# Optimization experiments

Hardware: AMD Instinct MI355X
Metric: run time of the kernel (lower is better)

The kernel has to match this reference:

```python
import jax, jax.numpy as jnp
import numpy as np

DIM = 1024
HIDDEN = 4096
N_EXPERTS = 8
K = 2
TEMP = 1.0


def setup_inputs() -> dict:
    key = jax.random.key(0)
    ks = jax.random.split(key, 7)
    s = 0.02
    x = jax.random.normal(ks[0], (4, 2048, DIM), dtype=jnp.float32)
    router_w = jax.random.normal(ks[1], (N_EXPERTS, DIM), dtype=jnp.float32) * s
    router_b = jnp.zeros((N_EXPERTS,), dtype=jnp.float32)
    # Expert(dim, hidden, 'swiglu'): fc1: dim -> 2*hidden, fc2: hidden -> dim
    w1 = jax.random.normal(ks[2], (N_EXPERTS, 2 * HIDDEN, DIM), dtype=jnp.float32) * s
    b1 = jnp.zeros((N_EXPERTS, 2 * HIDDEN), dtype=jnp.float32)
    w2 = jax.random.normal(ks[3], (N_EXPERTS, DIM, HIDDEN), dtype=jnp.float32) * s
    b2 = jnp.zeros((N_EXPERTS, DIM), dtype=jnp.float32)
    return {"x": x, "router_w": router_w, "router_b": router_b,
            "w1": w1, "b1": b1, "w2": w2, "b2": b2}


def _expert_ffn(xf, wa, ba, wb, bb):
    # xf: [T, dim]; swiglu FFN
    h = xf @ wa.T + ba                       # [T, 2*hidden]
    h1, h2 = jnp.split(h, 2, axis=-1)
    h = jax.nn.silu(h1) * h2                 # [T, hidden]
    return h @ wb.T + bb                     # [T, dim]


def reference(x, router_w, router_b, w1, b1, w2, b2):
    b, t, d = x.shape
    logits = (x @ router_w.T + router_b) / TEMP          # [b, t, E]
    topk_val, topk_idx = jax.lax.top_k(logits, K)        # [b, t, K]
    weights = jax.nn.softmax(topk_val, axis=-1)          # [b, t, K]

    xf = x.reshape(-1, d)                                # [T, dim]
    # Compute every expert on all tokens (dense reference for irregular dispatch)
    outs = jax.vmap(_expert_ffn, in_axes=(None, 0, 0, 0, 0))(xf, w1, b1, w2, b2)  # [E, T, dim]
    outs = jnp.transpose(outs, (1, 0, 2))                # [T, E, dim]

    idx = topk_idx.reshape(-1, K)                        # [T, K]
    gathered = jnp.take_along_axis(outs, idx[:, :, None], axis=1)  # [T, K, dim]
    combined = (gathered * weights.reshape(-1, K, 1)).sum(axis=1)  # [T, dim]
    return combined.reshape(b, t, d)
```

## Files before the change

### kernel.cpp

```cpp
#include <hip/hip_runtime.h>

#define T_TOK 8192
#define DIMX 1024
#define HID 4096
#define NE 8
#define TP (T_TOK * 2)
#define PADR 128
#define BK 64

typedef unsigned short ushort_t;
typedef __attribute__((ext_vector_type(4))) float f32x4;
typedef __attribute__((ext_vector_type(8))) short bf16x8;
typedef __attribute__((ext_vector_type(8))) unsigned short u16x8;

__device__ __forceinline__ ushort_t f2bf(float f) {
    unsigned u = __float_as_uint(f);
    u += 0x7FFFu + ((u >> 16) & 1u);
    return (ushort_t)(u >> 16);
}
__device__ __forceinline__ float b2f(ushort_t h) {
    return __uint_as_float(((unsigned)h) << 16);
}

__device__ __forceinline__ void gload_lds16(const void* g, void* l) {
    __builtin_amdgcn_global_load_lds((const __attribute__((address_space(1))) void*)g,
                                     (__attribute__((address_space(3))) void*)l, 16, 0, 0);
}

__device__ __forceinline__ f32x4 mfma16(bf16x8 a, bf16x8 b, f32x4 c) {
    return __builtin_amdgcn_mfma_f32_16x16x32_bf16(a, b, c, 0, 0, 0);
}


__global__ __launch_bounds__(256) void router_kernel(
    const float* __restrict__ x, const float* __restrict__ rw, const float* __restrict__ rb,
    int* __restrict__ topk_idx, float* __restrict__ topk_w)
{
    __shared__ float s_rw[NE * DIMX];
    int tid = threadIdx.x;
    for (int i = tid * 4; i < NE * DIMX; i += 1024) {
        float4 v = *(const float4*)(rw + i);
        *(float4*)(s_rw + i) = v;
    }
    __syncthreads();
    int lane = tid & 63, wid = tid >> 6;
    int t = blockIdx.x * 4 + wid;
    const float* xr = x + (size_t)t * DIMX;
    float acc[NE];
#pragma unroll
    for (int e = 0; e < NE; e++) acc[e] = 0.f;
    for (int j = 0; j < DIMX; j += 64) {
        float xv = xr[j + lane];
#pragma unroll
        for (int e = 0; e < NE; e++) acc[e] += xv * s_rw[e * DIMX + j + lane];
    }
#pragma unroll
    for (int e = 0; e < NE; e++) {
#pragma unroll
        for (int off = 32; off > 0; off >>= 1) acc[e] += __shfl_xor(acc[e], off, 64);
    }
    if (lane == 0) {
        float v[NE];
#pragma unroll
        for (int e = 0; e < NE; e++) v[e] = acc[e] + rb[e];
        int i0 = 0; float b0 = v[0];
#pragma unroll
        for (int e = 1; e < NE; e++) if (v[e] > b0) { b0 = v[e]; i0 = e; }
        int i1 = -1; float b1v = -1e30f;
#pragma unroll
        for (int e = 0; e < NE; e++) if (e != i0 && v[e] > b1v) { b1v = v[e]; i1 = e; }
        float ex = __expf(b1v - b0);
        float inv = 1.f / (1.f + ex);
        topk_idx[t * 2]     = i0;  topk_idx[t * 2 + 1] = i1;
        topk_w[t * 2]       = inv; topk_w[t * 2 + 1]   = ex * inv;
    }
}

__global__ __launch_bounds__(256) void prefix_kernel(
    const int* __restrict__ topk_idx, int* __restrict__ counts,
    int* __restrict__ offsets, int* __restrict__ cursor)
{
    __shared__ int hist[NE * 256];
    int tid = threadIdx.x;
    int loc[NE];
#pragma unroll
    for (int e = 0; e < NE; e++) loc[e] = 0;
    for (int i = tid; i < TP; i += 256) loc[topk_idx[i]]++;
#pragma unroll
    for (int e = 0; e < NE; e++) hist[e * 256 + tid] = loc[e];
    __syncthreads();
    if (tid < NE) {
        int s = 0;
        for (int j = 0; j < 256; j++) s += hist[tid * 256 + j];
        counts[tid] = s;
        cursor[tid] = 0;
    }
    __syncthreads();
    if (tid == 0) {
        int s = 0;
        for (int e = 0; e < NE; e++) { offsets[e] = s; s += counts[e]; }
    }
}

__global__ __launch_bounds__(256) void sg_kernel(
    const float* __restrict__ x, const int* __restrict__ topk_idx,
    const float* __restrict__ topk_w, const int* __restrict__ offsets,
    int* __restrict__ cursor, ushort_t* __restrict__ Xp,
    float* __restrict__ w_of, int* __restrict__ slot_of)
{
    __shared__ int s_pos[2];
    int t = blockIdx.x;
    if (threadIdx.x == 0) {
        int e0 = topk_idx[2 * t], e1 = topk_idx[2 * t + 1];
        int p0 = offsets[e0] + atomicAdd(&cursor[e0], 1);
        int p1 = offsets[e1] + atomicAdd(&cursor[e1], 1);
        s_pos[0] = p0; s_pos[1] = p1;
        w_of[p0] = topk_w[2 * t]; w_of[p1] = topk_w[2 * t + 1];
        slot_of[2 * t] = p0; slot_of[2 * t + 1] = p1;
    }
    __syncthreads();
    int p0 = s_pos[0], p1 = s_pos[1];
    int i = threadIdx.x;
    float4 v = ((const float4*)(x + (size_t)t * DIMX))[i];
    ushort4 o = make_ushort4(f2bf(v.x), f2bf(v.y), f2bf(v.z), f2bf(v.w));
    ((ushort4*)(Xp + (size_t)p0 * DIMX))[i] = o;
    ((ushort4*)(Xp + (size_t)p1 * DIMX))[i] = o;
}


__global__ __launch_bounds__(256) void cvt_kernel(
    const float* __restrict__ w1, ushort_t* __restrict__ w1d,
    const float* __restrict__ w2, ushort_t* __restrict__ w2d)
{
    const int n8_w1 = NE * 2 * HID * DIMX / 8;
    const int n8_tot = n8_w1 + NE * DIMX * HID / 8;
    int stride = gridDim.x * 256;
    for (int i = blockIdx.x * 256 + threadIdx.x; i < n8_tot; i += stride) {
        const float* src; ushort_t* dst; int j;
        if (i < n8_w1) { src = w1; dst = w1d; j = i; }
        else           { src = w2; dst = w2d; j = i - n8_w1; }
        float4 a = ((const float4*)src)[j * 2];
        float4 b = ((const float4*)src)[j * 2 + 1];
        u16x8 o = { f2bf(a.x), f2bf(a.y), f2bf(a.z), f2bf(a.w),
                    f2bf(b.x), f2bf(b.y), f2bf(b.z), f2bf(b.w) };
        ((u16x8*)dst)[j] = o;
    }
}

__global__ __launch_bounds__(256, 2) void fc1_kernel(
    const ushort_t* __restrict__ Xp, const ushort_t* __restrict__ w1b,
    const float* __restrict__ b1,
    const int* __restrict__ counts, const int* __restrict__ offsets,
    ushort_t* __restrict__ H, const int nt0)
{
    const int e = blockIdx.z, mt = blockIdx.y, nt = blockIdx.x + nt0;
    const int cnt = counts[e];
    if (mt * 128 >= cnt) return;
    const int base = offsets[e] + mt * 128;
    int rows_valid = cnt - mt * 128; if (rows_valid > 128) rows_valid = 128;

    __shared__ ushort_t As[128 * BK];
    __shared__ ushort_t Bs1[64 * BK];
    __shared__ ushort_t Bs2[64 * BK];

    const int tid = threadIdx.x, lane = tid & 63, wid = tid >> 6;
    const int wave_m = wid >> 1, wave_n = wid & 1;

    const ushort_t* Ag  = Xp + (size_t)base * DIMX;
    const ushort_t* B1g = w1b + ((size_t)e * 2 * HID + (size_t)nt * 64) * DIMX;
    const ushort_t* B2g = B1g + (size_t)HID * DIMX;

    const ushort_t* agp[4]; ushort_t* alp[4];
#pragma unroll
    for (int i = 0; i < 4; i++) {
        int s = wid * 4 + i;
        int r = s * 8 + (lane >> 3);
        int c = (lane & 7) ^ (r & 7);
        agp[i] = Ag + (size_t)r * DIMX + c * 8;
        alp[i] = As + s * 512 + lane * 8;
    }
    const ushort_t* bgp[4]; ushort_t* blp[4];
#pragma unroll
    for (int i = 0; i < 2; i++) {
        int s = wid * 2 + i;
        int r = s * 8 + (lane >> 3);
        int c = (lane & 7) ^ (r & 7);
        bgp[i]     = B1g + (size_t)r * DIMX + c * 8;
        blp[i]     = Bs1 + s * 512 + lane * 8;
        bgp[2 + i] = B2g + (size_t)r * DIMX + c * 8;
        blp[2 + i] = Bs2 + s * 512 + lane * 8;
    }

    f32x4 acc1[4][2], acc2[4][2];
#pragma unroll
    for (int mf = 0; mf < 4; mf++)
#pragma unroll
        for (int nf = 0; nf < 2; nf++) {
            acc1[mf][nf] = (f32x4){0.f, 0.f, 0.f, 0.f};
            acc2[mf][nf] = (f32x4){0.f, 0.f, 0.f, 0.f};
        }

    const int q = lane >> 4, rA = lane & 15;
    for (int ko = 0; ko < DIMX / BK; ko++) {
#pragma unroll
        for (int i = 0; i < 4; i++) gload_lds16(agp[i], alp[i]);
#pragma unroll
        for (int i = 0; i < 4; i++) gload_lds16(bgp[i], blp[i]);
#pragma unroll
        for (int i = 0; i < 4; i++) { agp[i] += BK; bgp[i] += BK; }
        __syncthreads();

        bf16x8 af[4][2], bf1[2][2], bf2[2][2];
#pragma unroll
        for (int mf = 0; mf < 4; mf++) {
            int r = wave_m * 64 + mf * 16 + rA;
            const ushort_t* rp = As + r * BK;
            af[mf][0] = *(const bf16x8*)(rp + ((q    ) ^ (r & 7)) * 8);
            af[mf][1] = *(const bf16x8*)(rp + ((q + 4) ^ (r & 7)) * 8);
        }
#pragma unroll
        for (int nf = 0; nf < 2; nf++) {
            int r = wave_n * 32 + nf * 16 + rA;
            const ushort_t* rp1 = Bs1 + r * BK;
            const ushort_t* rp2 = Bs2 + r * BK;
            bf1[nf][0] = *(const bf16x8*)(rp1 + ((q    ) ^ (r & 7)) * 8);
            bf1[nf][1] = *(const bf16x8*)(rp1 + ((q + 4) ^ (r & 7)) * 8);
            bf2[nf][0] = *(const bf16x8*)(rp2 + ((q    ) ^ (r & 7)) * 8);
            bf2[nf][1] = *(const bf16x8*)(rp2 + ((q + 4) ^ (r & 7)) * 8);
        }
#pragma unroll
        for (int mf = 0; mf < 4; mf++)
#pragma unroll
            for (int nf = 0; nf < 2; nf++) {
                acc1[mf][nf] = mfma16(af[mf][0], bf1[nf][0], acc1[mf][nf]);
                acc1[mf][nf] = mfma16(af[mf][1], bf1[nf][1], acc1[mf][nf]);
                acc2[mf][nf] = mfma16(af[mf][0], bf2[nf][0], acc2[mf][nf]);
                acc2[mf][nf] = mfma16(af[mf][1], bf2[nf][1], acc2[mf][nf]);
            }
        __syncthreads();
    }

    const float* b1p = b1 + (size_t)e * 2 * HID + (size_t)nt * 64;
    const bool full = (rows_valid == 128);
#pragma unroll
    for (int mf = 0; mf < 4; mf++) {
#pragma unroll
        for (int nf = 0; nf < 2; nf++) {
            int col = wave_n * 32 + nf * 16 + rA;
            float bb1 = b1p[col];
            float bb2 = b1p[HID + col];
#pragma unroll
            for (int rr = 0; rr < 4; rr++) {
                int row = wave_m * 64 + mf * 16 + q * 4 + rr;
                if (full || row < rows_valid) {
                    float v1 = acc1[mf][nf][rr] + bb1;
                    float v2 = acc2[mf][nf][rr] + bb2;
                    float hv = v1 * v2 / (1.f + __expf(-v1));
                    H[(size_t)(base + row) * HID + (size_t)nt * 64 + col] = f2bf(hv);
                }
            }
        }
    }
}

__global__ __launch_bounds__(256, 2) void fc2_kernel(
    const ushort_t* __restrict__ H, const ushort_t* __restrict__ w2b,
    const float* __restrict__ b2,
    const int* __restrict__ counts, const int* __restrict__ offsets,
    const float* __restrict__ w_of, ushort_t* __restrict__ Os)
{
    const int e = blockIdx.z, mt = blockIdx.x, nt = blockIdx.y;
    const int cnt = counts[e];
    if (mt * 128 >= cnt) return;
    const int base = offsets[e] + mt * 128;
    int rows_valid = cnt - mt * 128; if (rows_valid > 128) rows_valid = 128;

    __shared__ ushort_t As[128 * BK];
    __shared__ ushort_t Bs[128 * BK];

    const int tid = threadIdx.x, lane = tid & 63, wid = tid >> 6;
    const int wave_m = wid >> 1, wave_n = wid & 1;

    const ushort_t* Ag = H + (size_t)base * HID;
    const ushort_t* Bg = w2b + ((size_t)e * DIMX + (size_t)nt * 128) * HID;

    const ushort_t* agp[4]; ushort_t* alp[4];
    const ushort_t* bgp[4]; ushort_t* blp[4];
#pragma unroll
    for (int i = 0; i < 4; i++) {
        int s = wid * 4 + i;
        int r = s * 8 + (lane >> 3);
        int c = (lane & 7) ^ (r & 7);
        agp[i] = Ag + (size_t)r * HID + c * 8;
        alp[i] = As + s * 512 + lane * 8;
        bgp[i] = Bg + (size_t)r * HID + c * 8;
        blp[i] = Bs + s * 512 + lane * 8;
    }

    f32x4 acc[4][4];
#pragma unroll
    for (int mf = 0; mf < 4; mf++)
#pragma unroll
        for (int nf = 0; nf < 4; nf++) acc[mf][nf] = (f32x4){0.f, 0.f, 0.f, 0.f};

    const int q = lane >> 4, rA = lane & 15;
    for (int ko = 0; ko < HID / BK; ko++) {
#pragma unroll
        for (int i = 0; i < 4; i++) gload_lds16(agp[i], alp[i]);
#pragma unroll
        for (int i = 0; i < 4; i++) gload_lds16(bgp[i], blp[i]);
#pragma unroll
        for (int i = 0; i < 4; i++) { agp[i] += BK; bgp[i] += BK; }
        __syncthreads();

        bf16x8 af[4][2], bfr[4][2];
#pragma unroll
        for (int mf = 0; mf < 4; mf++) {
            int r = wave_m * 64 + mf * 16 + rA;
            const ushort_t* rp = As + r * BK;
            af[mf][0] = *(const bf16x8*)(rp + ((q    ) ^ (r & 7)) * 8);
            af[mf][1] = *(const bf16x8*)(rp + ((q + 4) ^ (r & 7)) * 8);
        }
#pragma unroll
        for (int nf = 0; nf < 4; nf++) {
            int r = wave_n * 64 + nf * 16 + rA;
            const ushort_t* rp = Bs + r * BK;
            bfr[nf][0] = *(const bf16x8*)(rp + ((q    ) ^ (r & 7)) * 8);
            bfr[nf][1] = *(const bf16x8*)(rp + ((q + 4) ^ (r & 7)) * 8);
        }
#pragma unroll
        for (int mf = 0; mf < 4; mf++)
#pragma unroll
            for (int nf = 0; nf < 4; nf++) {
                acc[mf][nf] = mfma16(af[mf][0], bfr[nf][0], acc[mf][nf]);
                acc[mf][nf] = mfma16(af[mf][1], bfr[nf][1], acc[mf][nf]);
            }
        __syncthreads();
    }

    const float* b2p = b2 + (size_t)e * DIMX + (size_t)nt * 128;
    const bool full = (rows_valid == 128);
#pragma unroll
    for (int mf = 0; mf < 4; mf++) {
#pragma unroll
        for (int rr = 0; rr < 4; rr++) {
            int row = wave_m * 64 + mf * 16 + q * 4 + rr;
            if (full || row < rows_valid) {
                float wv = w_of[base + row];
#pragma unroll
                for (int nf = 0; nf < 4; nf++) {
                    int col = wave_n * 64 + nf * 16 + rA;
                    float val = (acc[mf][nf][rr] + b2p[col]) * wv;
                    Os[(size_t)(base + row) * DIMX + (size_t)nt * 128 + col] = f2bf(val);
                }
            }
        }
    }
}

__global__ __launch_bounds__(256) void combine_kernel(
    const ushort_t* __restrict__ Os, const int* __restrict__ slot_of, float* __restrict__ out)
{
    int t = blockIdx.x;
    int p0 = slot_of[t * 2], p1 = slot_of[t * 2 + 1];
    int i = threadIdx.x;
    ushort4 a = ((const ushort4*)(Os + (size_t)p0 * DIMX))[i];
    ushort4 b = ((const ushort4*)(Os + (size_t)p1 * DIMX))[i];
    float4 o;
    o.x = b2f(a.x) + b2f(b.x);
    o.y = b2f(a.y) + b2f(b.y);
    o.z = b2f(a.z) + b2f(b.z);
    o.w = b2f(a.w) + b2f(b.w);
    ((float4*)(out + (size_t)t * DIMX))[i] = o;
}


extern "C" void kernel_launch(void* const* d_in, const int* in_sizes, int n_in,
                              void* d_out, int out_size, void* d_ws, size_t ws_size,
                              hipStream_t stream) {
    (void)in_sizes; (void)n_in; (void)out_size; (void)ws_size;
    const float* x  = (const float*)d_in[0];
    const float* rw = (const float*)d_in[1];
    const float* rb = (const float*)d_in[2];
    const float* w1 = (const float*)d_in[3];
    const float* b1 = (const float*)d_in[4];
    const float* w2 = (const float*)d_in[5];
    const float* b2 = (const float*)d_in[6];
    float* out = (float*)d_out;

    char* p = (char*)d_ws;
    ushort_t* w1b = (ushort_t*)p; p += (size_t)NE * 2 * HID * DIMX * 2;
    ushort_t* w2b = (ushort_t*)p; p += (size_t)NE * DIMX * HID * 2;
    ushort_t* Xp  = (ushort_t*)p; p += (size_t)(TP + PADR) * DIMX * 2;
    ushort_t* Hb  = (ushort_t*)p; p += (size_t)(TP + PADR) * HID * 2;
    int* ints     = (int*)p;      p += 24 * sizeof(int);
    int*   counts  = ints;
    int*   cursor  = ints + 8;
    int*   offsets = ints + 16;
    int*   topk_idx = (int*)p;   p += (size_t)TP * 4;
    float* topk_w   = (float*)p; p += (size_t)TP * 4;
    float* w_of     = (float*)p; p += (size_t)TP * 4;
    int*   slot_of  = (int*)p;   p += (size_t)TP * 4;
    ushort_t* Os = Xp;

    router_kernel<<<T_TOK / 4, 256, 0, stream>>>(x, rw, rb, topk_idx, topk_w);
    prefix_kernel<<<1, 256, 0, stream>>>(topk_idx, counts, offsets, cursor);
    sg_kernel<<<T_TOK, 256, 0, stream>>>(x, topk_idx, topk_w, offsets, cursor,
                                         Xp, w_of, slot_of);
    cvt_kernel<<<2048, 256, 0, stream>>>(w1, w1b, w2, w2b);

    fc1_kernel<<<dim3(32, 32, NE), 256, 0, stream>>>(Xp, w1b, b1, counts, offsets, Hb, 0);
    fc1_kernel<<<dim3(32, 32, NE), 256, 0, stream>>>(Xp, w1b, b1, counts, offsets, Hb, 32);
    fc2_kernel<<<dim3(32, DIMX / 128, NE), 256, 0, stream>>>(Hb, w2b, b2, counts, offsets, w_of, Os);
    combine_kernel<<<T_TOK, 256, 0, stream>>>(Os, slot_of, out);
}
```

Before: 1.317 ms.

## Rewrite expert GEMMs as 256x256 tiles with double-buffered LDS pipeline

Both expert GEMM kernels move from 128-row tiles with 256 threads and a single LDS buffer to 256x256 tiles with 512 threads. The K loop is split into 32-wide half-stages held in a double-buffered LDS layout, so global-to-LDS prefetch of the next stage overlaps the MFMA work through manual vmcnt waits, raw barriers and setprio. fc1 now interleaves the gate and up rows of w1 inside a single B tile, and the token padding is raised to cover the larger row tile. The aim is more data reuse per tile and hidden memory latency, at the cost of more registers and shared memory per block, fewer blocks, and fragile hand-written synchronisation.

```diff
diff --git a/kernel.cpp b/kernel.cpp
--- a/kernel.cpp
+++ b/kernel.cpp
@@ -5,7 +5,7 @@
 #define HID 4096
 #define NE 8
 #define TP (T_TOK * 2)
-#define PADR 128
+#define PADR 256
 #define BK 64
 
 typedef unsigned short ushort_t;
@@ -29,6 +29,10 @@
 
 __device__ __forceinline__ f32x4 mfma16(bf16x8 a, bf16x8 b, f32x4 c) {
     return __builtin_amdgcn_mfma_f32_16x16x32_bf16(a, b, c, 0, 0, 0);
+}
+
+__device__ __forceinline__ bf16x8 lds_frag(const ushort_t* sl, int row, int q) {
+    return *(const bf16x8*)(sl + row * 32 + (((q) ^ ((row >> 1) & 3)) << 3));
 }
 
 
@@ -147,123 +151,134 @@
     }
 }
 
-__global__ __launch_bounds__(256, 2) void fc1_kernel(
+
+#define STAGE_A(KS, KN, SN) do { \
+    gload_lds16(ag0 + (KN) + (KS) * 32, &As[(SN) * 16384 + (KS) * 8192 + adst0]); \
+    gload_lds16(ag1 + (KN) + (KS) * 32, &As[(SN) * 16384 + (KS) * 8192 + adst1]); } while (0)
+#define STAGE_B(KS, KN, SN) do { \
+    gload_lds16(bg0 + (KN) + (KS) * 32, &Bs[(SN) * 16384 + (KS) * 8192 + adst0]); \
+    gload_lds16(bg1 + (KN) + (KS) * 32, &Bs[(SN) * 16384 + (KS) * 8192 + adst1]); } while (0)
+
+#define PH_SYNC_COMPUTE(ACCBASE)                                            \
+    asm volatile("s_barrier" ::: "memory");                                 \
+    asm volatile("s_waitcnt lgkmcnt(0)" ::: "memory");                      \
+    __builtin_amdgcn_s_setprio(1);                                          \
+    _Pragma("unroll")                                                       \
+    for (int i = 0; i < 4; i++)                                             \
+        _Pragma("unroll")                                                   \
+        for (int j = 0; j < 4; j++)                                         \
+            acc[(ACCBASE) + i][j] = mfma16(af[i], bfr[j], acc[(ACCBASE) + i][j]); \
+    __builtin_amdgcn_s_setprio(0);
+
+__global__ __launch_bounds__(512, 2) void fc1_kernel(
     const ushort_t* __restrict__ Xp, const ushort_t* __restrict__ w1b,
     const float* __restrict__ b1,
     const int* __restrict__ counts, const int* __restrict__ offsets,
     ushort_t* __restrict__ H, const int nt0)
 {
-    const int e = blockIdx.z, mt = blockIdx.y, nt = blockIdx.x + nt0;
+    const int e = blockIdx.z, mt = blockIdx.x, nt = blockIdx.y + nt0;
     const int cnt = counts[e];
-    if (mt * 128 >= cnt) return;
-    const int base = offsets[e] + mt * 128;
-    int rows_valid = cnt - mt * 128; if (rows_valid > 128) rows_valid = 128;
-
-    __shared__ ushort_t As[128 * BK];
-    __shared__ ushort_t Bs1[64 * BK];
-    __shared__ ushort_t Bs2[64 * BK];
+    if (mt * 256 >= cnt) return;
+    const int base = offsets[e] + mt * 256;
+    int rows_valid = cnt - mt * 256; if (rows_valid > 256) rows_valid = 256;
+
+    __shared__ ushort_t As[2 * 2 * 256 * 32];
+    __shared__ ushort_t Bs[2 * 2 * 256 * 32];
 
     const int tid = threadIdx.x, lane = tid & 63, wid = tid >> 6;
-    const int wave_m = wid >> 1, wave_n = wid & 1;
-
+    const int wave_m = wid >> 2, wave_n = wid & 3;
+    const int wrow0 = wave_m * 128, wcol0 = wave_n * 64;
+    const int q = lane >> 4, rA = lane & 15;
+
+    const int r0 = wid * 32 + (lane >> 2);
+    const int cs = (lane & 3) ^ ((r0 >> 1) & 3);
     const ushort_t* Ag  = Xp + (size_t)base * DIMX;
-    const ushort_t* B1g = w1b + ((size_t)e * 2 * HID + (size_t)nt * 64) * DIMX;
-    const ushort_t* B2g = B1g + (size_t)HID * DIMX;
-
-    const ushort_t* agp[4]; ushort_t* alp[4];
-#pragma unroll
-    for (int i = 0; i < 4; i++) {
-        int s = wid * 4 + i;
-        int r = s * 8 + (lane >> 3);
-        int c = (lane & 7) ^ (r & 7);
-        agp[i] = Ag + (size_t)r * DIMX + c * 8;
-        alp[i] = As + s * 512 + lane * 8;
-    }
-    const ushort_t* bgp[4]; ushort_t* blp[4];
-#pragma unroll
-    for (int i = 0; i < 2; i++) {
-        int s = wid * 2 + i;
-        int r = s * 8 + (lane >> 3);
-        int c = (lane & 7) ^ (r & 7);
-        bgp[i]     = B1g + (size_t)r * DIMX + c * 8;
-        blp[i]     = Bs1 + s * 512 + lane * 8;
-        bgp[2 + i] = B2g + (size_t)r * DIMX + c * 8;
-        blp[2 + i] = Bs2 + s * 512 + lane * 8;
-    }
-
-    f32x4 acc1[4][2], acc2[4][2];
-#pragma unroll
-    for (int mf = 0; mf < 4; mf++)
-#pragma unroll
-        for (int nf = 0; nf < 2; nf++) {
-            acc1[mf][nf] = (f32x4){0.f, 0.f, 0.f, 0.f};
-            acc2[mf][nf] = (f32x4){0.f, 0.f, 0.f, 0.f};
-        }
-
-    const int q = lane >> 4, rA = lane & 15;
-    for (int ko = 0; ko < DIMX / BK; ko++) {
-#pragma unroll
-        for (int i = 0; i < 4; i++) gload_lds16(agp[i], alp[i]);
-#pragma unroll
-        for (int i = 0; i < 4; i++) gload_lds16(bgp[i], blp[i]);
-#pragma unroll
-        for (int i = 0; i < 4; i++) { agp[i] += BK; bgp[i] += BK; }
-        __syncthreads();
-
-        bf16x8 af[4][2], bf1[2][2], bf2[2][2];
-#pragma unroll
-        for (int mf = 0; mf < 4; mf++) {
-            int r = wave_m * 64 + mf * 16 + rA;
-            const ushort_t* rp = As + r * BK;
-            af[mf][0] = *(const bf16x8*)(rp + ((q    ) ^ (r & 7)) * 8);
-            af[mf][1] = *(const bf16x8*)(rp + ((q + 4) ^ (r & 7)) * 8);
-        }
-#pragma unroll
-        for (int nf = 0; nf < 2; nf++) {
-            int r = wave_n * 32 + nf * 16 + rA;
-            const ushort_t* rp1 = Bs1 + r * BK;
-            const ushort_t* rp2 = Bs2 + r * BK;
-            bf1[nf][0] = *(const bf16x8*)(rp1 + ((q    ) ^ (r & 7)) * 8);
-            bf1[nf][1] = *(const bf16x8*)(rp1 + ((q + 4) ^ (r & 7)) * 8);
-            bf2[nf][0] = *(const bf16x8*)(rp2 + ((q    ) ^ (r & 7)) * 8);
-            bf2[nf][1] = *(const bf16x8*)(rp2 + ((q + 4) ^ (r & 7)) * 8);
-        }
-#pragma unroll
-        for (int mf = 0; mf < 4; mf++)
-#pragma unroll
-            for (int nf = 0; nf < 2; nf++) {
-                acc1[mf][nf] = mfma16(af[mf][0], bf1[nf][0], acc1[mf][nf]);
-                acc1[mf][nf] = mfma16(af[mf][1], bf1[nf][1], acc1[mf][nf]);
-                acc2[mf][nf] = mfma16(af[mf][0], bf2[nf][0], acc2[mf][nf]);
-                acc2[mf][nf] = mfma16(af[mf][1], bf2[nf][1], acc2[mf][nf]);
-            }
-        __syncthreads();
-    }
-
-    const float* b1p = b1 + (size_t)e * 2 * HID + (size_t)nt * 64;
-    const bool full = (rows_valid == 128);
-#pragma unroll
-    for (int mf = 0; mf < 4; mf++) {
-#pragma unroll
-        for (int nf = 0; nf < 2; nf++) {
-            int col = wave_n * 32 + nf * 16 + rA;
-            float bb1 = b1p[col];
-            float bb2 = b1p[HID + col];
-#pragma unroll
-            for (int rr = 0; rr < 4; rr++) {
-                int row = wave_m * 64 + mf * 16 + q * 4 + rr;
-                if (full || row < rows_valid) {
-                    float v1 = acc1[mf][nf][rr] + bb1;
-                    float v2 = acc2[mf][nf][rr] + bb2;
+    const ushort_t* ag0 = Ag + (size_t)r0 * DIMX + cs * 8;
+    const ushort_t* ag1 = Ag + (size_t)(r0 + 16) * DIMX + cs * 8;
+    const ushort_t* Bg  = w1b + (size_t)e * 2 * HID * DIMX;
+    const int g0 = nt * 128 + wid * 16 + (lane >> 2);
+    const ushort_t* bg0 = Bg + (size_t)g0 * DIMX + cs * 8;
+    const ushort_t* bg1 = Bg + (size_t)(HID + g0) * DIMX + cs * 8;
+    const int adst0 = wid * 1024 + lane * 8;
+    const int adst1 = adst0 + 512;
+
+    f32x4 acc[8][4];
+#pragma unroll
+    for (int mf = 0; mf < 8; mf++)
+#pragma unroll
+        for (int nf = 0; nf < 4; nf++) acc[mf][nf] = (f32x4){0.f, 0.f, 0.f, 0.f};
+
+    STAGE_A(0, 0, 0); STAGE_B(0, 0, 0); STAGE_A(1, 0, 0); STAGE_B(1, 0, 0);
+    asm volatile("s_waitcnt vmcnt(4)" ::: "memory");
+    asm volatile("s_barrier" ::: "memory");
+
+    const int NKT = DIMX / BK;
+#pragma unroll 2
+    for (int kt = 0; kt < NKT; ++kt) {
+        const int sl = kt & 1, sn = sl ^ 1;
+        const ushort_t* A0 = &As[sl * 16384];
+        const ushort_t* A1 = A0 + 8192;
+        const ushort_t* B0 = &Bs[sl * 16384];
+        const ushort_t* B1 = B0 + 8192;
+        const bool pf = (kt + 1 < NKT);
+        const int kn = (kt + 1) * BK;
+
+        bf16x8 af[4], bfr[4];
+#pragma unroll
+        for (int j = 0; j < 4; j++) bfr[j] = lds_frag(B0, wcol0 + j * 16 + rA, q);
+#pragma unroll
+        for (int i = 0; i < 4; i++) af[i] = lds_frag(A0, wrow0 + i * 16 + rA, q);
+        if (pf) STAGE_A(0, kn, sn);
+        PH_SYNC_COMPUTE(0)
+        asm volatile("s_barrier" ::: "memory");
+
+#pragma unroll
+        for (int i = 0; i < 4; i++) af[i] = lds_frag(A0, wrow0 + 64 + i * 16 + rA, q);
+        if (pf) STAGE_B(0, kn, sn);
+        PH_SYNC_COMPUTE(4)
+        if (pf) { asm volatile("s_waitcnt vmcnt(4)" ::: "memory"); }
+        else    { asm volatile("s_waitcnt vmcnt(0)" ::: "memory"); }
+        asm volatile("s_barrier" ::: "memory");
+
+#pragma unroll
+        for (int j = 0; j < 4; j++) bfr[j] = lds_frag(B1, wcol0 + j * 16 + rA, q);
+#pragma unroll
+        for (int i = 0; i < 4; i++) af[i] = lds_frag(A1, wrow0 + i * 16 + rA, q);
+        if (pf) STAGE_A(1, kn, sn);
+        PH_SYNC_COMPUTE(0)
+        asm volatile("s_barrier" ::: "memory");
+
+#pragma unroll
+        for (int i = 0; i < 4; i++) af[i] = lds_frag(A1, wrow0 + 64 + i * 16 + rA, q);
+        if (pf) STAGE_B(1, kn, sn);
+        PH_SYNC_COMPUTE(4)
+        if (pf) { asm volatile("s_waitcnt vmcnt(4)" ::: "memory"); }
+        else    { asm volatile("s_waitcnt vmcnt(0)" ::: "memory"); }
+        asm volatile("s_barrier" ::: "memory");
+    }
+
+    const float* b1p = b1 + (size_t)e * 2 * HID;
+    const bool full = (rows_valid == 256);
+#pragma unroll
+    for (int mf = 0; mf < 8; mf++) {
+#pragma unroll
+        for (int rr = 0; rr < 4; rr++) {
+            int row = wrow0 + mf * 16 + q * 4 + rr;
+            if (full || row < rows_valid) {
+#pragma unroll
+                for (int nfp = 0; nfp < 2; nfp++) {
+                    int hcol = nt * 128 + (wave_n * 2 + nfp) * 16 + rA;
+                    float v1 = acc[mf][2 * nfp][rr] + b1p[hcol];
+                    float v2 = acc[mf][2 * nfp + 1][rr] + b1p[HID + hcol];
                     float hv = v1 * v2 / (1.f + __expf(-v1));
-                    H[(size_t)(base + row) * HID + (size_t)nt * 64 + col] = f2bf(hv);
+                    H[(size_t)(base + row) * HID + hcol] = f2bf(hv);
                 }
             }
         }
     }
 }
 
-__global__ __launch_bounds__(256, 2) void fc2_kernel(
+__global__ __launch_bounds__(512, 2) void fc2_kernel(
     const ushort_t* __restrict__ H, const ushort_t* __restrict__ w2b,
     const float* __restrict__ b2,
     const int* __restrict__ counts, const int* __restrict__ offsets,
@@ -271,87 +286,98 @@
 {
     const int e = blockIdx.z, mt = blockIdx.x, nt = blockIdx.y;
     const int cnt = counts[e];
-    if (mt * 128 >= cnt) return;
-    const int base = offsets[e] + mt * 128;
-    int rows_valid = cnt - mt * 128; if (rows_valid > 128) rows_valid = 128;
-
-    __shared__ ushort_t As[128 * BK];
-    __shared__ ushort_t Bs[128 * BK];
+    if (mt * 256 >= cnt) return;
+    const int base = offsets[e] + mt * 256;
+    int rows_valid = cnt - mt * 256; if (rows_valid > 256) rows_valid = 256;
+
+    __shared__ ushort_t As[2 * 2 * 256 * 32];
+    __shared__ ushort_t Bs[2 * 2 * 256 * 32];
 
     const int tid = threadIdx.x, lane = tid & 63, wid = tid >> 6;
-    const int wave_m = wid >> 1, wave_n = wid & 1;
-
-    const ushort_t* Ag = H + (size_t)base * HID;
-    const ushort_t* Bg = w2b + ((size_t)e * DIMX + (size_t)nt * 128) * HID;
-
-    const ushort_t* agp[4]; ushort_t* alp[4];
-    const ushort_t* bgp[4]; ushort_t* blp[4];
-#pragma unroll
-    for (int i = 0; i < 4; i++) {
-        int s = wid * 4 + i;
-        int r = s * 8 + (lane >> 3);
-        int c = (lane & 7) ^ (r & 7);
-        agp[i] = Ag + (size_t)r * HID + c * 8;
-        alp[i] = As + s * 512 + lane * 8;
-        bgp[i] = Bg + (size_t)r * HID + c * 8;
-        blp[i] = Bs + s * 512 + lane * 8;
-    }
-
-    f32x4 acc[4][4];
-#pragma unroll
-    for (int mf = 0; mf < 4; mf++)
+    const int wave_m = wid >> 2, wave_n = wid & 3;
+    const int wrow0 = wave_m * 128, wcol0 = wave_n * 64;
+    const int q = lane >> 4, rA = lane & 15;
+
+    const int r0 = wid * 32 + (lane >> 2);
+    const int cs = (lane & 3) ^ ((r0 >> 1) & 3);
+    const ushort_t* Ag  = H + (size_t)base * HID;
+    const ushort_t* ag0 = Ag + (size_t)r0 * HID + cs * 8;
+    const ushort_t* ag1 = Ag + (size_t)(r0 + 16) * HID + cs * 8;
+    const ushort_t* Bg  = w2b + (size_t)e * DIMX * HID;
+    const ushort_t* bg0 = Bg + (size_t)(nt * 256 + r0) * HID + cs * 8;
+    const ushort_t* bg1 = Bg + (size_t)(nt * 256 + r0 + 16) * HID + cs * 8;
+    const int adst0 = wid * 1024 + lane * 8;
+    const int adst1 = adst0 + 512;
+
+    f32x4 acc[8][4];
+#pragma unroll
+    for (int mf = 0; mf < 8; mf++)
 #pragma unroll
         for (int nf = 0; nf < 4; nf++) acc[mf][nf] = (f32x4){0.f, 0.f, 0.f, 0.f};
 
-    const int q = lane >> 4, rA = lane & 15;
-    for (int ko = 0; ko < HID / BK; ko++) {
-#pragma unroll
-        for (int i = 0; i < 4; i++) gload_lds16(agp[i], alp[i]);
-#pragma unroll
-        for (int i = 0; i < 4; i++) gload_lds16(bgp[i], blp[i]);
-#pragma unroll
-        for (int i = 0; i < 4; i++) { agp[i] += BK; bgp[i] += BK; }
-        __syncthreads();
-
-        bf16x8 af[4][2], bfr[4][2];
-#pragma unroll
-        for (int mf = 0; mf < 4; mf++) {
-            int r = wave_m * 64 + mf * 16 + rA;
-            const ushort_t* rp = As + r * BK;
-            af[mf][0] = *(const bf16x8*)(rp + ((q    ) ^ (r & 7)) * 8);
-            af[mf][1] = *(const bf16x8*)(rp + ((q + 4) ^ (r & 7)) * 8);
-        }
-#pragma unroll
-        for (int nf = 0; nf < 4; nf++) {
-            int r = wave_n * 64 + nf * 16 + rA;
-            const ushort_t* rp = Bs + r * BK;
-            bfr[nf][0] = *(const bf16x8*)(rp + ((q    ) ^ (r & 7)) * 8);
-            bfr[nf][1] = *(const bf16x8*)(rp + ((q + 4) ^ (r & 7)) * 8);
-        }
-#pragma unroll
-        for (int mf = 0; mf < 4; mf++)
-#pragma unroll
-            for (int nf = 0; nf < 4; nf++) {
-                acc[mf][nf] = mfma16(af[mf][0], bfr[nf][0], acc[mf][nf]);
-                acc[mf][nf] = mfma16(af[mf][1], bfr[nf][1], acc[mf][nf]);
-            }
-        __syncthreads();
-    }
-
-    const float* b2p = b2 + (size_t)e * DIMX + (size_t)nt * 128;
-    const bool full = (rows_valid == 128);
-#pragma unroll
-    for (int mf = 0; mf < 4; mf++) {
+    STAGE_A(0, 0, 0); STAGE_B(0, 0, 0); STAGE_A(1, 0, 0); STAGE_B(1, 0, 0);
+    asm volatile("s_waitcnt vmcnt(4)" ::: "memory");
+    asm volatile("s_barrier" ::: "memory");
+
+    const int NKT = HID / BK;
+#pragma unroll 2
+    for (int kt = 0; kt < NKT; ++kt) {
+        const int sl = kt & 1, sn = sl ^ 1;
+        const ushort_t* A0 = &As[sl * 16384];
+        const ushort_t* A1 = A0 + 8192;
+        const ushort_t* B0 = &Bs[sl * 16384];
+        const ushort_t* B1 = B0 + 8192;
+        const bool pf = (kt + 1 < NKT);
+        const int kn = (kt + 1) * BK;
+
+        bf16x8 af[4], bfr[4];
+#pragma unroll
+        for (int j = 0; j < 4; j++) bfr[j] = lds_frag(B0, wcol0 + j * 16 + rA, q);
+#pragma unroll
+        for (int i = 0; i < 4; i++) af[i] = lds_frag(A0, wrow0 + i * 16 + rA, q);
+        if (pf) STAGE_A(0, kn, sn);
+        PH_SYNC_COMPUTE(0)
+        asm volatile("s_barrier" ::: "memory");
+
+#pragma unroll
+        for (int i = 0; i < 4; i++) af[i] = lds_frag(A0, wrow0 + 64 + i * 16 + rA, q);
+        if (pf) STAGE_B(0, kn, sn);
+        PH_SYNC_COMPUTE(4)
+        if (pf) { asm volatile("s_waitcnt vmcnt(4)" ::: "memory"); }
+        else    { asm volatile("s_waitcnt vmcnt(0)" ::: "memory"); }
+        asm volatile("s_barrier" ::: "memory");
+
+#pragma unroll
+        for (int j = 0; j < 4; j++) bfr[j] = lds_frag(B1, wcol0 + j * 16 + rA, q);
+#pragma unroll
+        for (int i = 0; i < 4; i++) af[i] = lds_frag(A1, wrow0 + i * 16 + rA, q);
+        if (pf) STAGE_A(1, kn, sn);
+        PH_SYNC_COMPUTE(0)
+        asm volatile("s_barrier" ::: "memory");
+
+#pragma unroll
+        for (int i = 0; i < 4; i++) af[i] = lds_frag(A1, wrow0 + 64 + i * 16 + rA, q);
+        if (pf) STAGE_B(1, kn, sn);
+        PH_SYNC_COMPUTE(4)
+        if (pf) { asm volatile("s_waitcnt vmcnt(4)" ::: "memory"); }
+        else    { asm volatile("s_waitcnt vmcnt(0)" ::: "memory"); }
+        asm volatile("s_barrier" ::: "memory");
+    }
+
+    const float* b2p = b2 + (size_t)e * DIMX + (size_t)nt * 256;
+    const bool full = (rows_valid == 256);
+#pragma unroll
+    for (int mf = 0; mf < 8; mf++) {
 #pragma unroll
         for (int rr = 0; rr < 4; rr++) {
-            int row = wave_m * 64 + mf * 16 + q * 4 + rr;
+            int row = wrow0 + mf * 16 + q * 4 + rr;
             if (full || row < rows_valid) {
                 float wv = w_of[base + row];
 #pragma unroll
                 for (int nf = 0; nf < 4; nf++) {
-                    int col = wave_n * 64 + nf * 16 + rA;
+                    int col = wcol0 + nf * 16 + rA;
                     float val = (acc[mf][nf][rr] + b2p[col]) * wv;
-                    Os[(size_t)(base + row) * DIMX + (size_t)nt * 128 + col] = f2bf(val);
+                    Os[(size_t)(base + row) * DIMX + (size_t)nt * 256 + col] = f2bf(val);
                 }
             }
         }
@@ -409,8 +435,8 @@
                                          Xp, w_of, slot_of);
     cvt_kernel<<<2048, 256, 0, stream>>>(w1, w1b, w2, w2b);
 
-    fc1_kernel<<<dim3(32, 32, NE), 256, 0, stream>>>(Xp, w1b, b1, counts, offsets, Hb, 0);
-    fc1_kernel<<<dim3(32, 32, NE), 256, 0, stream>>>(Xp, w1b, b1, counts, offsets, Hb, 32);
-    fc2_kernel<<<dim3(32, DIMX / 128, NE), 256, 0, stream>>>(Hb, w2b, b2, counts, offsets, w_of, Os);
+    fc1_kernel<<<dim3(32, 16, NE), 512, 0, stream>>>(Xp, w1b, b1, counts, offsets, Hb, 0);
+    fc1_kernel<<<dim3(32, 16, NE), 512, 0, stream>>>(Xp, w1b, b1, counts, offsets, Hb, 16);
+    fc2_kernel<<<dim3(32, DIMX / 256, NE), 512, 0, stream>>>(Hb, w2b, b2, counts, offsets, w_of, Os);
     combine_kernel<<<T_TOK, 256, 0, stream>>>(Os, slot_of, out);
 }
```

Result: slower. 2.520 ms (+91.4%).
